# Performance work log

Hardware: AMD Instinct MI355X
Metric: run time of the kernel (lower is better)

## Reference

```python
import jax, jax.numpy as jnp
import numpy as np

BSZ, L, D = 8, 2048, 1024

def setup_inputs() -> dict:
    key = jax.random.key(0)
    k1, k2, k3, k4 = jax.random.split(key, 4)
    s = 1.0 / np.sqrt(D)
    return {
        "x":   jax.random.normal(k1, (BSZ, L, D), dtype=jnp.float32),
        "A":   jax.random.normal(k2, (D,), dtype=jnp.float32),
        "W_B": jax.random.normal(k3, (D, D), dtype=jnp.float32) * s,
        "b_B": jnp.zeros((D,), dtype=jnp.float32),
        "W_C": jax.random.normal(k4, (D, D), dtype=jnp.float32) * s,
        "b_C": jnp.zeros((D,), dtype=jnp.float32),
    }

def reference(x, A, W_B, b_B, W_C, b_C):
    # Precompute B(x_t) for all t in one GEMM: [B, L, D]
    Bx = jnp.einsum("bld,ed->ble", x, W_B) + b_B
    h0 = jnp.zeros((x.shape[0], x.shape[2]), dtype=x.dtype)

    def step(h, bx_t):
        h = jnp.tanh(A * h + bx_t)   # elementwise recurrence
        return h, h

    # scan over time: Bx -> [L, B, D]
    _, hs = jax.lax.scan(step, h0, jnp.swapaxes(Bx, 0, 1))
    # y_t = C(h_t), batched over all t: hs [L, B, D]
    y = jnp.einsum("lbd,ed->lbe", hs, W_C) + b_C
    return jnp.swapaxes(y, 0, 1)  # [B, L, D]
```

## Files before the change

kernel.cpp:

```cpp
#include <hip/hip_runtime.h>
#include <hip/hip_bf16.h>
#include <stdint.h>


using half8 = __attribute__((ext_vector_type(8))) _Float16;
using f32x4 = __attribute__((ext_vector_type(4))) float;

#define DEV __device__ __forceinline__

#if __has_builtin(__builtin_amdgcn_exp2f)
DEV float pexp(float x) { return __builtin_amdgcn_exp2f(x); }
constexpr float BX_SCALE = 2.8853900817779268f;
#else
DEV float pexp(float x) { return __expf(x); }
constexpr float BX_SCALE = 2.0f;
#endif

DEV ushort f2h(float x) {
  union { _Float16 f; ushort u; } c;
  c.f = (_Float16)x;
  return c.u;
}
DEV float h2f(ushort u) {
  union { ushort u; _Float16 f; } c;
  c.u = u;
  return (float)c.f;
}

DEV void gload_lds16(const void* g, void* l) {
  __builtin_amdgcn_global_load_lds((const __attribute__((address_space(1))) void*)g,
                                   (__attribute__((address_space(3))) void*)l,
                                   16, 0, 0);
}

__global__ void k_split_convert(const float* __restrict__ in, ushort* __restrict__ hi,
                                ushort* __restrict__ lo, int n4) {
  const int stride = gridDim.x * blockDim.x;
  for (int i = blockIdx.x * blockDim.x + threadIdx.x; i < n4; i += stride) {
    float4 v = reinterpret_cast<const float4*>(in)[i];
    ushort4 hv, lv;
    hv.x = f2h(v.x); lv.x = f2h(v.x - h2f(hv.x));
    hv.y = f2h(v.y); lv.y = f2h(v.y - h2f(hv.y));
    hv.z = f2h(v.z); lv.z = f2h(v.z - h2f(hv.z));
    hv.w = f2h(v.w); lv.w = f2h(v.w - h2f(hv.w));
    reinterpret_cast<ushort4*>(hi)[i] = hv;
    reinterpret_cast<ushort4*>(lo)[i] = lv;
  }
}

__global__ void k_convert(const float* __restrict__ in, ushort* __restrict__ out, int n4) {
  const int stride = gridDim.x * blockDim.x;
  for (int i = blockIdx.x * blockDim.x + threadIdx.x; i < n4; i += stride) {
    float4 v = reinterpret_cast<const float4*>(in)[i];
    ushort4 hv;
    hv.x = f2h(v.x); hv.y = f2h(v.y);
    hv.z = f2h(v.z); hv.w = f2h(v.w);
    reinterpret_cast<ushort4*>(out)[i] = hv;
  }
}

template <int SPLIT, int SCALE>
__global__ __launch_bounds__(256, 2)
void k_gemm_bt(const ushort* __restrict__ Ah, const ushort* __restrict__ Al,
               const ushort* __restrict__ Bh, const ushort* __restrict__ Bl,
               const float* __restrict__ bias, float* __restrict__ C,
               int M, int N, int K) {
  constexpr int NMAT = SPLIT ? 4 : 2;
  __shared__ __align__(1024) ushort lds[NMAT * 128 * 64];
  ushort* sAh = lds;
  ushort* sAl = lds + (SPLIT ? 8192 : 0);
  ushort* sBh = lds + (SPLIT ? 16384 : 8192);
  ushort* sBl = lds + (SPLIT ? 24576 : 8192);

  const int t = threadIdx.x;
  const int lane = t & 63;
  const int w = t >> 6;
  const int wm = w >> 1, wn = w & 1;

  int bm, bn;
  if (gridDim.x == 8) {
    const int l = blockIdx.y * 8 + blockIdx.x;
    const int xcd = l & 7, s = l >> 3;
    bm = ((s >> 3) << 3) | xcd;
    bn = s & 7;
  } else {
    bm = blockIdx.y; bn = blockIdx.x;
  }

  const int lr = lane & 15;
  const int lk = (lane >> 4) << 3;

  const ushort* gA_h = Ah + (size_t)(bm * 128) * K;
  const ushort* gA_l = SPLIT ? (Al + (size_t)(bm * 128) * K) : gA_h;
  const ushort* gB_h = Bh + (size_t)(bn * 128) * K;
  const ushort* gB_l = SPLIT ? (Bl + (size_t)(bn * 128) * K) : gB_h;

  f32x4 acc[4][4];
#pragma unroll
  for (int i = 0; i < 4; ++i)
#pragma unroll
    for (int j = 0; j < 4; ++j)
#pragma unroll
      for (int r = 0; r < 4; ++r) acc[i][j][r] = 0.f;

  auto stage = [&](int kt) {
    const int k0 = kt * 64;
#pragma unroll
    for (int i = 0; i < 4; ++i) {
      const int lin16 = i * 256 + t;
      const int lb = lin16 << 4;
      const int row = lb >> 7;
      const int srcb = (lb & 127) ^ ((row & 7) << 4);
      const size_t goff = (size_t)row * K + (size_t)(k0 + (srcb >> 1));
      const int lidx = i * 2048 + w * 512;
      gload_lds16(gA_h + goff, sAh + lidx);
      if (SPLIT) gload_lds16(gA_l + goff, sAl + lidx);
      gload_lds16(gB_h + goff, sBh + lidx);
      if (SPLIT) gload_lds16(gB_l + goff, sBl + lidx);
    }
  };

  auto ldfrag = [&](const ushort* s, int row, int kc) -> half8 {
    const int byte = (row << 7) + (((kc << 1) ^ ((row & 7) << 4)));
    return *reinterpret_cast<const half8*>(reinterpret_cast<const char*>(s) + byte);
  };

  const int NT = K / 64;
  stage(0);
  for (int kt = 0; kt < NT; ++kt) {
    __syncthreads();
#pragma unroll
    for (int kk = 0; kk < 2; ++kk) {
      half8 ah[4], bh[4], al[4], bl[4];
      const int kc = kk * 32 + lk;
#pragma unroll
      for (int i = 0; i < 4; ++i) {
        const int row = wm * 64 + i * 16 + lr;
        ah[i] = ldfrag(sAh, row, kc);
        if (SPLIT) al[i] = ldfrag(sAl, row, kc);
      }
#pragma unroll
      for (int j = 0; j < 4; ++j) {
        const int row = wn * 64 + j * 16 + lr;
        bh[j] = ldfrag(sBh, row, kc);
        if (SPLIT) bl[j] = ldfrag(sBl, row, kc);
      }
#pragma unroll
      for (int i = 0; i < 4; ++i)
#pragma unroll
        for (int j = 0; j < 4; ++j) {
          acc[i][j] = __builtin_amdgcn_mfma_f32_16x16x32_f16(ah[i], bh[j], acc[i][j], 0, 0, 0);
          if (SPLIT) {
            acc[i][j] = __builtin_amdgcn_mfma_f32_16x16x32_f16(al[i], bh[j], acc[i][j], 0, 0, 0);
            acc[i][j] = __builtin_amdgcn_mfma_f32_16x16x32_f16(ah[i], bl[j], acc[i][j], 0, 0, 0);
          }
        }
    }
    __syncthreads();
    if (kt + 1 < NT) stage(kt + 1);
  }

  float* Cb = C + (size_t)(bm * 128) * N + bn * 128;
#pragma unroll
  for (int i = 0; i < 4; ++i)
#pragma unroll
    for (int j = 0; j < 4; ++j) {
      const int col = wn * 64 + j * 16 + lr;
      const float bv = bias[bn * 128 + col];
#pragma unroll
      for (int r = 0; r < 4; ++r) {
        const int rowt = wm * 64 + i * 16 + ((lane >> 4) << 2) + r;
        float o = acc[i][j][r] + bv;
        if (SCALE) o *= BX_SCALE;
        Cb[(size_t)rowt * N + col] = o;
      }
    }
}

__global__ __launch_bounds__(64)
void k_recurrence(const float* __restrict__ Bx2, const float* __restrict__ Avec,
                  ushort* __restrict__ Hout) {
  const int tid = blockIdx.x * 64 + threadIdx.x;
  const int b = tid >> 10;
  const int d = tid & 1023;
  const float a2 = BX_SCALE * Avec[d];
  const float* bx = Bx2 + (size_t)b * 2048 * 1024 + d;
  ushort* ho = Hout + (size_t)b * 2048 * 1024 + d;

  constexpr int P = 32;
  constexpr int NC = 2048 / P;
  float bufA[P], bufB[P];
#pragma unroll
  for (int i = 0; i < P; ++i) bufA[i] = bx[(size_t)i * 1024];
#pragma unroll
  for (int i = 0; i < P; ++i) bufB[i] = bx[(size_t)(P + i) * 1024];

  float h = 0.f;
  for (int c = 0; c < NC; c += 2) {
#pragma unroll
    for (int i = 0; i < P; ++i) {
      const float u2 = fmaf(a2, h, bufA[i]);
      const float p  = pexp(u2);
      const float r  = __builtin_amdgcn_rcpf(p + 1.f);
      h = fmaf(-2.f, r, 1.f);
      ho[(size_t)(c * P + i) * 1024] = f2h(h);
    }
    if (c + 2 < NC) {
#pragma unroll
      for (int i = 0; i < P; ++i) bufA[i] = bx[(size_t)((c + 2) * P + i) * 1024];
    }
#pragma unroll
    for (int i = 0; i < P; ++i) {
      const float u2 = fmaf(a2, h, bufB[i]);
      const float p  = pexp(u2);
      const float r  = __builtin_amdgcn_rcpf(p + 1.f);
      h = fmaf(-2.f, r, 1.f);
      ho[(size_t)((c + 1) * P + i) * 1024] = f2h(h);
    }
    if (c + 3 < NC) {
#pragma unroll
      for (int i = 0; i < P; ++i) bufB[i] = bx[(size_t)((c + 3) * P + i) * 1024];
    }
  }
}

extern "C" void kernel_launch(void* const* d_in, const int* in_sizes, int n_in,
                              void* d_out, int out_size, void* d_ws, size_t ws_size,
                              hipStream_t stream) {
  const float* x   = (const float*)d_in[0];
  const float* A   = (const float*)d_in[1];
  const float* W_B = (const float*)d_in[2];
  const float* b_B = (const float*)d_in[3];
  const float* W_C = (const float*)d_in[4];
  const float* b_C = (const float*)d_in[5];
  float* y = (float*)d_out;

  const int Bsz = 8, L = 2048, D = 1024;
  const int M = Bsz * L;

  char* ws = (char*)d_ws;
  ushort* x_hi  = (ushort*)(ws);
  ushort* x_lo  = (ushort*)(ws + 33554432);
  ushort* wb_hi = (ushort*)(ws + 67108864);
  ushort* wb_lo = (ushort*)(ws + 69206016);
  ushort* wc    = (ushort*)(ws + 71303168);
  float*  Bx    = (float*)(ws + 73400320);
  ushort* h     = x_hi;

  k_split_convert<<<2048, 256, 0, stream>>>(x, x_hi, x_lo, M * D / 4);
  k_split_convert<<<512, 256, 0, stream>>>(W_B, wb_hi, wb_lo, D * D / 4);
  k_convert<<<512, 256, 0, stream>>>(W_C, wc, D * D / 4);

  k_gemm_bt<1, 1><<<dim3(D / 128, M / 128), 256, 0, stream>>>(
      x_hi, x_lo, wb_hi, wb_lo, b_B, Bx, M, D, D);

  k_recurrence<<<(Bsz * D) / 64, 64, 0, stream>>>(Bx, A, h);

  k_gemm_bt<0, 0><<<dim3(D / 128, M / 128), 256, 0, stream>>>(
      h, (const ushort*)nullptr, wc, (const ushort*)nullptr, b_C, y, M, D, D);
}
```

Baseline: 232.6 us.

## Fuse x fp32-to-split-fp16 conversion into first GEMM and merge weight conversions

Drops the standalone pass that split x into hi/lo fp16 arrays. The first GEMM now loads fp32 x tiles into registers, splits them into hi and lo halves and writes them to LDS, with the next tile's global load issued before the MFMA loop. This removes a full write and re-read of the 64 MB intermediate. The two weight conversion kernels become one launch. The recurrence is rewritten in terms of the sigmoid value r, folding a2 into the preloaded Bx so each step does one fewer FMA on the serial dependency chain. The cost is that A-tile conversion work and an extra barrier now sit inside the GEMM mainloop.

```diff
diff --git a/kernel.cpp b/kernel.cpp
--- a/kernel.cpp
+++ b/kernel.cpp
@@ -33,44 +33,40 @@
                                    16, 0, 0);
 }
 
-__global__ void k_split_convert(const float* __restrict__ in, ushort* __restrict__ hi,
-                                ushort* __restrict__ lo, int n4) {
+__global__ void k_convert_weights(const float* __restrict__ WB, const float* __restrict__ WC,
+                                  ushort* __restrict__ wbh, ushort* __restrict__ wbl,
+                                  ushort* __restrict__ wch, int n4) {
   const int stride = gridDim.x * blockDim.x;
-  for (int i = blockIdx.x * blockDim.x + threadIdx.x; i < n4; i += stride) {
-    float4 v = reinterpret_cast<const float4*>(in)[i];
-    ushort4 hv, lv;
-    hv.x = f2h(v.x); lv.x = f2h(v.x - h2f(hv.x));
-    hv.y = f2h(v.y); lv.y = f2h(v.y - h2f(hv.y));
-    hv.z = f2h(v.z); lv.z = f2h(v.z - h2f(hv.z));
-    hv.w = f2h(v.w); lv.w = f2h(v.w - h2f(hv.w));
-    reinterpret_cast<ushort4*>(hi)[i] = hv;
-    reinterpret_cast<ushort4*>(lo)[i] = lv;
-  }
-}
-
-__global__ void k_convert(const float* __restrict__ in, ushort* __restrict__ out, int n4) {
-  const int stride = gridDim.x * blockDim.x;
-  for (int i = blockIdx.x * blockDim.x + threadIdx.x; i < n4; i += stride) {
-    float4 v = reinterpret_cast<const float4*>(in)[i];
-    ushort4 hv;
-    hv.x = f2h(v.x); hv.y = f2h(v.y);
-    hv.z = f2h(v.z); hv.w = f2h(v.w);
-    reinterpret_cast<ushort4*>(out)[i] = hv;
-  }
-}
-
-template <int SPLIT, int SCALE>
+  for (int i = blockIdx.x * blockDim.x + threadIdx.x; i < 2 * n4; i += stride) {
+    if (i < n4) {
+      float4 v = reinterpret_cast<const float4*>(WB)[i];
+      ushort4 hv, lv;
+      hv.x = f2h(v.x); lv.x = f2h(v.x - h2f(hv.x));
+      hv.y = f2h(v.y); lv.y = f2h(v.y - h2f(hv.y));
+      hv.z = f2h(v.z); lv.z = f2h(v.z - h2f(hv.z));
+      hv.w = f2h(v.w); lv.w = f2h(v.w - h2f(hv.w));
+      reinterpret_cast<ushort4*>(wbh)[i] = hv;
+      reinterpret_cast<ushort4*>(wbl)[i] = lv;
+    } else {
+      const int j = i - n4;
+      float4 v = reinterpret_cast<const float4*>(WC)[j];
+      ushort4 hv;
+      hv.x = f2h(v.x); hv.y = f2h(v.y);
+      hv.z = f2h(v.z); hv.w = f2h(v.w);
+      reinterpret_cast<ushort4*>(wch)[j] = hv;
+    }
+  }
+}
+
 __global__ __launch_bounds__(256, 2)
-void k_gemm_bt(const ushort* __restrict__ Ah, const ushort* __restrict__ Al,
-               const ushort* __restrict__ Bh, const ushort* __restrict__ Bl,
-               const float* __restrict__ bias, float* __restrict__ C,
-               int M, int N, int K) {
-  constexpr int NMAT = SPLIT ? 4 : 2;
-  __shared__ __align__(1024) ushort lds[NMAT * 128 * 64];
+void k_gemm1_fused(const float* __restrict__ X, const ushort* __restrict__ Bh,
+                   const ushort* __restrict__ Bl, const float* __restrict__ bias,
+                   float* __restrict__ C, int M, int N, int K) {
+  __shared__ __align__(1024) ushort lds[4 * 128 * 64];
   ushort* sAh = lds;
-  ushort* sAl = lds + (SPLIT ? 8192 : 0);
-  ushort* sBh = lds + (SPLIT ? 16384 : 8192);
-  ushort* sBl = lds + (SPLIT ? 24576 : 8192);
+  ushort* sAl = lds + 8192;
+  ushort* sBh = lds + 16384;
+  ushort* sBl = lds + 24576;
 
   const int t = threadIdx.x;
   const int lane = t & 63;
@@ -78,22 +74,19 @@
   const int wm = w >> 1, wn = w & 1;
 
   int bm, bn;
-  if (gridDim.x == 8) {
+  {
     const int l = blockIdx.y * 8 + blockIdx.x;
     const int xcd = l & 7, s = l >> 3;
     bm = ((s >> 3) << 3) | xcd;
     bn = s & 7;
-  } else {
-    bm = blockIdx.y; bn = blockIdx.x;
   }
 
   const int lr = lane & 15;
   const int lk = (lane >> 4) << 3;
 
-  const ushort* gA_h = Ah + (size_t)(bm * 128) * K;
-  const ushort* gA_l = SPLIT ? (Al + (size_t)(bm * 128) * K) : gA_h;
-  const ushort* gB_h = Bh + (size_t)(bn * 128) * K;
-  const ushort* gB_l = SPLIT ? (Bl + (size_t)(bn * 128) * K) : gB_h;
+  const float*  gA  = X  + (size_t)(bm * 128) * K;
+  const ushort* gBh = Bh + (size_t)(bn * 128) * K;
+  const ushort* gBl = Bl + (size_t)(bn * 128) * K;
 
   f32x4 acc[4][4];
 #pragma unroll
@@ -103,7 +96,36 @@
 #pragma unroll
       for (int r = 0; r < 4; ++r) acc[i][j][r] = 0.f;
 
-  auto stage = [&](int kt) {
+  float4 areg[8];
+
+  auto issueA = [&](int kt) {
+    const int k0 = kt * 64;
+#pragma unroll
+    for (int j = 0; j < 8; ++j) {
+      const int g = j * 256 + t;
+      const int row = g >> 4;
+      const int cf = (g & 15) << 2;
+      areg[j] = *reinterpret_cast<const float4*>(gA + (size_t)row * K + k0 + cf);
+    }
+  };
+  auto writeA = [&]() {
+#pragma unroll
+    for (int j = 0; j < 8; ++j) {
+      const int g = j * 256 + t;
+      const int row = g >> 4;
+      const int cb2 = (g & 15) << 3;
+      const float4 v = areg[j];
+      ushort4 hv, lv;
+      hv.x = f2h(v.x); lv.x = f2h(v.x - h2f(hv.x));
+      hv.y = f2h(v.y); lv.y = f2h(v.y - h2f(hv.y));
+      hv.z = f2h(v.z); lv.z = f2h(v.z - h2f(hv.z));
+      hv.w = f2h(v.w); lv.w = f2h(v.w - h2f(hv.w));
+      const int off = (row << 7) + (cb2 ^ ((row & 7) << 4));
+      *reinterpret_cast<ushort4*>(reinterpret_cast<char*>(sAh) + off) = hv;
+      *reinterpret_cast<ushort4*>(reinterpret_cast<char*>(sAl) + off) = lv;
+    }
+  };
+  auto stageB = [&](int kt) {
     const int k0 = kt * 64;
 #pragma unroll
     for (int i = 0; i < 4; ++i) {
@@ -113,15 +135,118 @@
       const int srcb = (lb & 127) ^ ((row & 7) << 4);
       const size_t goff = (size_t)row * K + (size_t)(k0 + (srcb >> 1));
       const int lidx = i * 2048 + w * 512;
-      gload_lds16(gA_h + goff, sAh + lidx);
-      if (SPLIT) gload_lds16(gA_l + goff, sAl + lidx);
-      gload_lds16(gB_h + goff, sBh + lidx);
-      if (SPLIT) gload_lds16(gB_l + goff, sBl + lidx);
-    }
-  };
-
+      gload_lds16(gBh + goff, sBh + lidx);
+      gload_lds16(gBl + goff, sBl + lidx);
+    }
+  };
   auto ldfrag = [&](const ushort* s, int row, int kc) -> half8 {
-    const int byte = (row << 7) + (((kc << 1) ^ ((row & 7) << 4)));
+    const int byte = (row << 7) + ((kc << 1) ^ ((row & 7) << 4));
+    return *reinterpret_cast<const half8*>(reinterpret_cast<const char*>(s) + byte);
+  };
+
+  const int NT = K / 64;
+  stageB(0);
+  issueA(0);
+  writeA();
+  __syncthreads();
+  for (int kt = 0; kt < NT; ++kt) {
+    if (kt + 1 < NT) issueA(kt + 1);
+#pragma unroll
+    for (int kk = 0; kk < 2; ++kk) {
+      half8 ah[4], al[4], bh[4], bl[4];
+      const int kc = kk * 32 + lk;
+#pragma unroll
+      for (int i = 0; i < 4; ++i) {
+        const int r = wm * 64 + i * 16 + lr;
+        ah[i] = ldfrag(sAh, r, kc);
+        al[i] = ldfrag(sAl, r, kc);
+      }
+#pragma unroll
+      for (int j = 0; j < 4; ++j) {
+        const int r = wn * 64 + j * 16 + lr;
+        bh[j] = ldfrag(sBh, r, kc);
+        bl[j] = ldfrag(sBl, r, kc);
+      }
+#pragma unroll
+      for (int i = 0; i < 4; ++i)
+#pragma unroll
+        for (int j = 0; j < 4; ++j) {
+          acc[i][j] = __builtin_amdgcn_mfma_f32_16x16x32_f16(ah[i], bh[j], acc[i][j], 0, 0, 0);
+          acc[i][j] = __builtin_amdgcn_mfma_f32_16x16x32_f16(al[i], bh[j], acc[i][j], 0, 0, 0);
+          acc[i][j] = __builtin_amdgcn_mfma_f32_16x16x32_f16(ah[i], bl[j], acc[i][j], 0, 0, 0);
+        }
+    }
+    __syncthreads();
+    if (kt + 1 < NT) { stageB(kt + 1); writeA(); }
+    __syncthreads();
+  }
+
+  float* Cb = C + (size_t)(bm * 128) * N + bn * 128;
+#pragma unroll
+  for (int i = 0; i < 4; ++i)
+#pragma unroll
+    for (int j = 0; j < 4; ++j) {
+      const int col = wn * 64 + j * 16 + lr;
+      const float bv = bias[bn * 128 + col];
+#pragma unroll
+      for (int r = 0; r < 4; ++r) {
+        const int rowt = wm * 64 + i * 16 + ((lane >> 4) << 2) + r;
+        Cb[(size_t)rowt * N + col] = (acc[i][j][r] + bv) * BX_SCALE;
+      }
+    }
+}
+
+__global__ __launch_bounds__(256, 2)
+void k_gemm2(const ushort* __restrict__ Ah, const ushort* __restrict__ Bh,
+             const float* __restrict__ bias, float* __restrict__ C,
+             int M, int N, int K) {
+  __shared__ __align__(1024) ushort lds[2 * 128 * 64];
+  ushort* sAh = lds;
+  ushort* sBh = lds + 8192;
+
+  const int t = threadIdx.x;
+  const int lane = t & 63;
+  const int w = t >> 6;
+  const int wm = w >> 1, wn = w & 1;
+
+  int bm, bn;
+  {
+    const int l = blockIdx.y * 8 + blockIdx.x;
+    const int xcd = l & 7, s = l >> 3;
+    bm = ((s >> 3) << 3) | xcd;
+    bn = s & 7;
+  }
+
+  const int lr = lane & 15;
+  const int lk = (lane >> 4) << 3;
+
+  const ushort* gA = Ah + (size_t)(bm * 128) * K;
+  const ushort* gB = Bh + (size_t)(bn * 128) * K;
+
+  f32x4 acc[4][4];
+#pragma unroll
+  for (int i = 0; i < 4; ++i)
+#pragma unroll
+    for (int j = 0; j < 4; ++j)
+#pragma unroll
+      for (int r = 0; r < 4; ++r) acc[i][j][r] = 0.f;
+
+  auto stage = [&](int kt) {
+    const int k0 = kt * 64;
+#pragma unroll
+    for (int i = 0; i < 4; ++i) {
+      const int lin16 = i * 256 + t;
+      const int lb = lin16 << 4;
+      const int row = lb >> 7;
+      const int srcb = (lb & 127) ^ ((row & 7) << 4);
+      const size_t goff = (size_t)row * K + (size_t)(k0 + (srcb >> 1));
+      const int lidx = i * 2048 + w * 512;
+      gload_lds16(gA + goff, sAh + lidx);
+      gload_lds16(gB + goff, sBh + lidx);
+    }
+  };
+  auto ldfrag = [&](const ushort* s, int row, int kc) -> half8 {
+    const int byte = (row << 7) + ((kc << 1) ^ ((row & 7) << 4));
     return *reinterpret_cast<const half8*>(reinterpret_cast<const char*>(s) + byte);
   };
 
@@ -131,30 +256,17 @@
     __syncthreads();
 #pragma unroll
     for (int kk = 0; kk < 2; ++kk) {
-      half8 ah[4], bh[4], al[4], bl[4];
+      half8 ah[4], bh[4];
       const int kc = kk * 32 + lk;
 #pragma unroll
-      for (int i = 0; i < 4; ++i) {
-        const int row = wm * 64 + i * 16 + lr;
-        ah[i] = ldfrag(sAh, row, kc);
-        if (SPLIT) al[i] = ldfrag(sAl, row, kc);
-      }
-#pragma unroll
-      for (int j = 0; j < 4; ++j) {
-        const int row = wn * 64 + j * 16 + lr;
-        bh[j] = ldfrag(sBh, row, kc);
-        if (SPLIT) bl[j] = ldfrag(sBl, row, kc);
-      }
+      for (int i = 0; i < 4; ++i) ah[i] = ldfrag(sAh, wm * 64 + i * 16 + lr, kc);
+#pragma unroll
+      for (int j = 0; j < 4; ++j) bh[j] = ldfrag(sBh, wn * 64 + j * 16 + lr, kc);
 #pragma unroll
       for (int i = 0; i < 4; ++i)
 #pragma unroll
-        for (int j = 0; j < 4; ++j) {
+        for (int j = 0; j < 4; ++j)
           acc[i][j] = __builtin_amdgcn_mfma_f32_16x16x32_f16(ah[i], bh[j], acc[i][j], 0, 0, 0);
-          if (SPLIT) {
-            acc[i][j] = __builtin_amdgcn_mfma_f32_16x16x32_f16(al[i], bh[j], acc[i][j], 0, 0, 0);
-            acc[i][j] = __builtin_amdgcn_mfma_f32_16x16x32_f16(ah[i], bl[j], acc[i][j], 0, 0, 0);
-          }
-        }
     }
     __syncthreads();
     if (kt + 1 < NT) stage(kt + 1);
@@ -170,9 +282,7 @@
 #pragma unroll
       for (int r = 0; r < 4; ++r) {
         const int rowt = wm * 64 + i * 16 + ((lane >> 4) << 2) + r;
-        float o = acc[i][j][r] + bv;
-        if (SCALE) o *= BX_SCALE;
-        Cb[(size_t)rowt * N + col] = o;
+        Cb[(size_t)rowt * N + col] = acc[i][j][r] + bv;
       }
     }
 }
@@ -184,42 +294,39 @@
   const int b = tid >> 10;
   const int d = tid & 1023;
   const float a2 = BX_SCALE * Avec[d];
+  const float na2 = -2.f * a2;
   const float* bx = Bx2 + (size_t)b * 2048 * 1024 + d;
   ushort* ho = Hout + (size_t)b * 2048 * 1024 + d;
 
   constexpr int P = 32;
   constexpr int NC = 2048 / P;
-  float bufA[P], bufB[P];
-#pragma unroll
-  for (int i = 0; i < P; ++i) bufA[i] = bx[(size_t)i * 1024];
-#pragma unroll
-  for (int i = 0; i < P; ++i) bufB[i] = bx[(size_t)(P + i) * 1024];
-
-  float h = 0.f;
+  float cA[P], cB[P];
+#pragma unroll
+  for (int i = 0; i < P; ++i) cA[i] = a2 + bx[(size_t)i * 1024];
+#pragma unroll
+  for (int i = 0; i < P; ++i) cB[i] = a2 + bx[(size_t)(P + i) * 1024];
+
+  float r = 0.5f;
   for (int c = 0; c < NC; c += 2) {
 #pragma unroll
     for (int i = 0; i < P; ++i) {
-      const float u2 = fmaf(a2, h, bufA[i]);
-      const float p  = pexp(u2);
-      const float r  = __builtin_amdgcn_rcpf(p + 1.f);
-      h = fmaf(-2.f, r, 1.f);
-      ho[(size_t)(c * P + i) * 1024] = f2h(h);
+      const float u2 = fmaf(na2, r, cA[i]);
+      r = __builtin_amdgcn_rcpf(pexp(u2) + 1.f);
+      ho[(size_t)(c * P + i) * 1024] = f2h(fmaf(-2.f, r, 1.f));
     }
     if (c + 2 < NC) {
 #pragma unroll
-      for (int i = 0; i < P; ++i) bufA[i] = bx[(size_t)((c + 2) * P + i) * 1024];
+      for (int i = 0; i < P; ++i) cA[i] = a2 + bx[(size_t)((c + 2) * P + i) * 1024];
     }
 #pragma unroll
     for (int i = 0; i < P; ++i) {
-      const float u2 = fmaf(a2, h, bufB[i]);
-      const float p  = pexp(u2);
-      const float r  = __builtin_amdgcn_rcpf(p + 1.f);
-      h = fmaf(-2.f, r, 1.f);
-      ho[(size_t)((c + 1) * P + i) * 1024] = f2h(h);
+      const float u2 = fmaf(na2, r, cB[i]);
+      r = __builtin_amdgcn_rcpf(pexp(u2) + 1.f);
+      ho[(size_t)((c + 1) * P + i) * 1024] = f2h(fmaf(-2.f, r, 1.f));
     }
     if (c + 3 < NC) {
 #pragma unroll
-      for (int i = 0; i < P; ++i) bufB[i] = bx[(size_t)((c + 3) * P + i) * 1024];
+      for (int i = 0; i < P; ++i) cB[i] = a2 + bx[(size_t)((c + 3) * P + i) * 1024];
     }
   }
 }
@@ -239,23 +346,19 @@
   const int M = Bsz * L;
 
   char* ws = (char*)d_ws;
-  ushort* x_hi  = (ushort*)(ws);
-  ushort* x_lo  = (ushort*)(ws + 33554432);
-  ushort* wb_hi = (ushort*)(ws + 67108864);
-  ushort* wb_lo = (ushort*)(ws + 69206016);
-  ushort* wc    = (ushort*)(ws + 71303168);
-  float*  Bx    = (float*)(ws + 73400320);
-  ushort* h     = x_hi;
-
-  k_split_convert<<<2048, 256, 0, stream>>>(x, x_hi, x_lo, M * D / 4);
-  k_split_convert<<<512, 256, 0, stream>>>(W_B, wb_hi, wb_lo, D * D / 4);
-  k_convert<<<512, 256, 0, stream>>>(W_C, wc, D * D / 4);
-
-  k_gemm_bt<1, 1><<<dim3(D / 128, M / 128), 256, 0, stream>>>(
-      x_hi, x_lo, wb_hi, wb_lo, b_B, Bx, M, D, D);
+  ushort* wbh = (ushort*)(ws);
+  ushort* wbl = (ushort*)(ws + 2097152);
+  ushort* wch = (ushort*)(ws + 4194304);
+  float*  Bx  = (float*)(ws + 6291456);
+  ushort* h   = (ushort*)(ws + 73400320);
+
+  k_convert_weights<<<512, 256, 0, stream>>>(W_B, W_C, wbh, wbl, wch, D * D / 4);
+
+  k_gemm1_fused<<<dim3(8, M / 128), 256, 0, stream>>>(
+      x, wbh, wbl, b_B, Bx, M, D, D);
 
   k_recurrence<<<(Bsz * D) / 64, 64, 0, stream>>>(Bx, A, h);
 
-  k_gemm_bt<0, 0><<<dim3(D / 128, M / 128), 256, 0, stream>>>(
-      h, (const ushort*)nullptr, wc, (const ushort*)nullptr, b_C, y, M, D, D);
-}
+  k_gemm2<<<dim3(8, M / 128), 256, 0, stream>>>(
+      h, wch, b_C, y, M, D, D);
+}
```

Result: slower. 242.1 us (+4.1%).
